# Performance work log

Hardware: AMD Instinct MI355X
Metric: run time of the kernel (lower is better)

Reference implementation:

```python
import jax, jax.numpy as jnp
import numpy as np
import math

EPS = 1e-12
SUPPORT = 1  # support_num
NEIGHBOR_NUM = 32

def _l2norm(x, axis):
    n = jnp.sqrt(jnp.sum(x * x, axis=axis, keepdims=True))
    return x / jnp.maximum(n, EPS)

def _sq_dist(a, b):
    # a: (bs, v1, 3), b: (bs, v2, 3) -> (bs, v1, v2)
    inner = jnp.einsum('bic,bjc->bij', a, b)
    a2 = jnp.sum(a * a, axis=-1)
    b2 = jnp.sum(b * b, axis=-1)
    return a2[:, :, None] + b2[:, None, :] - 2.0 * inner

def _knn(verts, k):
    d = _sq_dist(verts, verts)
    _, idx = jax.lax.top_k(-d, k + 1)
    return idx[:, :, 1:]  # drop self

def _gather(t, idx):
    # t: (bs, v, d), idx: (bs, ...) -> (bs, ..., d)
    return jax.vmap(lambda ti, ii: ti[ii])(t, idx)

def _dir_theta(nb_idx, verts, directions):
    nbr = _gather(verts, nb_idx) - verts[:, :, None, :]  # (bs, v, n, 3)
    nbr = _l2norm(nbr, -1)
    sup = _l2norm(directions, 0)  # (3, s*out)
    return jax.nn.relu(jnp.einsum('bvnc,ck->bvnk', nbr, sup))

def _conv_surface(nb_idx, verts, directions, kernel_num):
    theta = _dir_theta(nb_idx, verts, directions)
    bs, v, n, _ = theta.shape
    theta = theta.reshape(bs, v, n, SUPPORT, kernel_num)
    return jnp.sum(jnp.max(theta, axis=2), axis=2)  # (bs, v, kernel)

def _conv_layer(nb_idx, verts, fm, w, b, directions, out_ch):
    theta = _dir_theta(nb_idx, verts, directions)  # (bs, v, n, s*out)
    f = fm @ w + b  # (bs, v, (s+1)*out)
    center = f[..., :out_ch]
    supp_nb = _gather(f[..., out_ch:], nb_idx)  # (bs, v, n, s*out)
    bs, v, n, _ = theta.shape
    act = (theta * supp_nb).reshape(bs, v, n, SUPPORT, out_ch)
    return center + jnp.sum(jnp.max(act, axis=2), axis=2)

def _pool(verts, fm, sample_idx, nbk=4):
    nb = _knn(verts, nbk)
    pooled = jnp.max(_gather(fm, nb), axis=2)
    return verts[:, sample_idx, :], pooled[:, sample_idx, :]

def _nearest(target, source):
    return jnp.argmin(_sq_dist(target, source), axis=-1)  # (bs, v1)

def _forward(vertices, sample_idx1, sample_idx2, dir0, w1, b1, d1, w2, b2, d2,
             w3, b3, d3, w4, b4, d4, cw1, cb1, cw2, cb2, cw3, cb3):
    nb = _knn(vertices, NEIGHBOR_NUM)
    fm_0 = jax.nn.relu(_conv_surface(nb, vertices, dir0, 128))
    fm_1 = jax.nn.relu(_conv_layer(nb, vertices, fm_0, w1, b1, d1, 128))
    v_p1, fm_p1 = _pool(vertices, fm_1, sample_idx1)
    nb = _knn(v_p1, NEIGHBOR_NUM)
    fm_2 = jax.nn.relu(_conv_layer(nb, v_p1, fm_p1, w2, b2, d2, 256))
    fm_3 = jax.nn.relu(_conv_layer(nb, v_p1, fm_2, w3, b3, d3, 256))
    v_p2, fm_p2 = _pool(v_p1, fm_3, sample_idx2)
    nb = _knn(v_p2, NEIGHBOR_NUM)
    fm_4 = _conv_layer(nb, v_p2, fm_p2, w4, b4, d4, 512)  # no relu
    f_global = jnp.max(fm_4, axis=1)  # (bs, 512)
    near1 = _nearest(vertices, v_p1)
    near2 = _nearest(vertices, v_p2)
    fm_2u = _gather(fm_2, near1)
    fm_3u = _gather(fm_3, near1)
    fm_4u = _gather(fm_4, near2)
    bs, v = vertices.shape[0], vertices.shape[1]
    fg = jnp.broadcast_to(f_global[:, None, :], (bs, v, f_global.shape[-1]))
    fuse = jnp.concatenate([fm_0, fm_1, fm_2u, fm_3u, fm_4u, fg], axis=2)  # (bs, v, 1792)
    h = jax.nn.relu(jnp.einsum('bvc,oc->bvo', fuse, cw1) + cb1)
    h = jax.nn.relu(jnp.einsum('bvc,oc->bvo', h, cw2) + cb2)
    return jnp.einsum('bvc,oc->bvo', h, cw3) + cb3  # (bs, v, class_num)


def setup_inputs() -> dict:
    key = jax.random.key(0)
    ks = jax.random.split(key, 24)
    BS, N, CLS = 4, 4096, 13
    def u(k, shape, s):
        return jax.random.uniform(k, shape, jnp.float32, -s, s)
    inp = {}
    inp['vertices'] = jax.random.normal(ks[0], (BS, N, 3), jnp.float32)
    inp['sample_idx1'] = jax.random.permutation(ks[1], N)[:N // 4]
    inp['sample_idx2'] = jax.random.permutation(ks[2], N // 4)[:N // 16]
    inp['dir0'] = u(ks[3], (3, SUPPORT * 128), 1.0 / math.sqrt(SUPPORT * 128))
    def conv_params(k1, k2, k3, cin, cout):
        s = 1.0 / math.sqrt(cout * (SUPPORT + 1))
        return (u(k1, (cin, (SUPPORT + 1) * cout), s),
                u(k2, ((SUPPORT + 1) * cout,), s),
                u(k3, (3, SUPPORT * cout), s))
    inp['w1'], inp['b1'], inp['d1'] = conv_params(ks[4], ks[5], ks[6], 128, 128)
    inp['w2'], inp['b2'], inp['d2'] = conv_params(ks[7], ks[8], ks[9], 128, 256)
    inp['w3'], inp['b3'], inp['d3'] = conv_params(ks[10], ks[11], ks[12], 256, 256)
    inp['w4'], inp['b4'], inp['d4'] = conv_params(ks[13], ks[14], ks[15], 256, 512)
    DF = 1792
    inp['cw1'] = u(ks[16], (512, DF), 1.0 / math.sqrt(DF))
    inp['cb1'] = u(ks[17], (512,), 1.0 / math.sqrt(DF))
    inp['cw2'] = u(ks[18], (512, 512), 1.0 / math.sqrt(512))
    inp['cb2'] = u(ks[19], (512,), 1.0 / math.sqrt(512))
    inp['cw3'] = u(ks[20], (CLS, 512), 1.0 / math.sqrt(512))
    inp['cb3'] = u(ks[21], (CLS,), 1.0 / math.sqrt(512))
    return inp


def reference(vertices, sample_idx1, sample_idx2, dir0, w1, b1, d1, w2, b2, d2,
              w3, b3, d3, w4, b4, d4, cw1, cb1, cw2, cb2, cw3, cb3):
    return _forward(vertices, sample_idx1, sample_idx2, dir0, w1, b1, d1, w2, b2, d2,
                    w3, b3, d3, w4, b4, d4, cw1, cb1, cw2, cb2, cw3, cb3)
```

## Files before the change

kernel.cpp:

```cpp
#include <hip/hip_runtime.h>
#include <cstdint>
#include <cstddef>

namespace {

typedef unsigned short ushort_t;
typedef __bf16 bf16x8 __attribute__((ext_vector_type(8)));
typedef float  f32x4  __attribute__((ext_vector_type(4)));

constexpr int B_ = 4;
constexpr int N0 = 4096;
constexpr int N1 = 1024;
constexpr int N2 = 256;

__device__ __forceinline__ ushort_t f2bf_rne(float x) {
  uint32_t b = __float_as_uint(x);
  b += 0x7FFFu + ((b >> 16) & 1u);
  return (ushort_t)(b >> 16);
}
__device__ __forceinline__ float bf2f(ushort_t h) {
  return __uint_as_float(((uint32_t)h) << 16);
}
__device__ __forceinline__ void split_store(float x, ushort_t* hi, ushort_t* lo,
                                            size_t i) {
  const ushort_t h = f2bf_rne(x);
  hi[i] = h;
  lo[i] = f2bf_rne(x - bf2f(h));
}

__global__ void weight_prep_kernel(
    const float* __restrict__ w1, const float* __restrict__ w2,
    const float* __restrict__ w3, const float* __restrict__ w4,
    const float* __restrict__ cw1, const float* __restrict__ cw2,
    ushort_t* __restrict__ w1th, ushort_t* __restrict__ w1tl,
    ushort_t* __restrict__ w2th, ushort_t* __restrict__ w2tl,
    ushort_t* __restrict__ w3th, ushort_t* __restrict__ w3tl,
    ushort_t* __restrict__ w4th, ushort_t* __restrict__ w4tl,
    ushort_t* __restrict__ w1h, ushort_t* __restrict__ w1l,
    ushort_t* __restrict__ w2h, ushort_t* __restrict__ w2l)
{
  const int i = blockIdx.x * blockDim.x + threadIdx.x;
  if (i < 32768) {
    const int j = i, k = j % 128, n = j / 128;
    split_store(w1[(size_t)k * 256 + n], w1th, w1tl, (size_t)n * 128 + k);
  } else if (i < 98304) {
    const int j = i - 32768, k = j % 128, n = j / 128;
    split_store(w2[(size_t)k * 512 + n], w2th, w2tl, (size_t)n * 128 + k);
  } else if (i < 229376) {
    const int j = i - 98304, k = j % 256, n = j / 256;
    split_store(w3[(size_t)k * 512 + n], w3th, w3tl, (size_t)n * 256 + k);
  } else if (i < 491520) {
    const int j = i - 229376, k = j % 256, n = j / 256;
    split_store(w4[(size_t)k * 1024 + n], w4th, w4tl, (size_t)n * 256 + k);
  } else if (i < 1409024) {
    const int j = i - 491520;
    split_store(cw1[j], w1h, w1l, j);
  } else if (i < 1671168) {
    const int j = i - 1409024;
    split_store(cw2[j], w2h, w2l, j);
  }
}

__device__ __forceinline__ void bitonic_sort64(float& sd, int& si, int lane) {
#pragma unroll
  for (int kk = 2; kk <= 64; kk <<= 1) {
#pragma unroll
    for (int j = kk >> 1; j > 0; j >>= 1) {
      const float od = __shfl_xor(sd, j);
      const int   oi = __shfl_xor(si, j);
      const bool less    = (sd < od) || (sd == od && si < oi);
      const bool wantMin = ((lane & j) == 0) == ((lane & kk) == 0);
      if (wantMin != less) { sd = od; si = oi; }
    }
  }
}

__device__ __forceinline__ void knn_flush(float& ld, int& li, float& tau,
                                          int cnt, const float* bufd,
                                          const int* bufi, int lane, int Km1) {
  float sd = (lane < cnt) ? bufd[lane] : INFINITY;
  int   si = (lane < cnt) ? bufi[lane] : 0x7fffffff;
  bitonic_sort64(sd, si, lane);
  const float rd = __shfl(sd, 63 - lane);
  const int   ri = __shfl(si, 63 - lane);
  const bool keep = (ld < rd) || (ld == rd && li < ri);
  float md = keep ? ld : rd;
  int   mi = keep ? li : ri;
#pragma unroll
  for (int j = 32; j > 0; j >>= 1) {
    const float od = __shfl_xor(md, j);
    const int   oi = __shfl_xor(mi, j);
    const bool less    = (md < od) || (md == od && mi < oi);
    const bool wantMin = ((lane & j) == 0);
    if (wantMin != less) { md = od; mi = oi; }
  }
  ld = md; li = mi;
  tau = __shfl(ld, Km1);
}

template<int K, int TILE>
__launch_bounds__(512)
__global__ void knn_wave_kernel(const float* __restrict__ pts,
                                int Q, int C,
                                int* __restrict__ out)
{
  __shared__ float4 sp[TILE];
  __shared__ float sbd[8][64];
  __shared__ int   sbi[8][64];
  const int b    = blockIdx.y;
  const int lane = threadIdx.x & 63;
  const int wid  = threadIdx.x >> 6;
  const int q    = blockIdx.x * 8 + wid;
  const int self = q;
  const float* pb = pts + (size_t)b * C * 3;
  const float qx = pb[self * 3 + 0];
  const float qy = pb[self * 3 + 1];
  const float qz = pb[self * 3 + 2];
  const float q2   = qx * qx + qy * qy + qz * qz;
  const float m2qx = -2.0f * qx, m2qy = -2.0f * qy, m2qz = -2.0f * qz;

  float ld = INFINITY; int li = 0x7fffffff;
  float tau = INFINITY;
  int cnt = 0;
  float* bufd = sbd[wid];
  int*   bufi = sbi[wid];

  auto append = [&](unsigned long long m, bool cand, float d, int ci) {
    const int c = __popcll(m);
    if (cnt + c > 64) {
      knn_flush(ld, li, tau, cnt, bufd, bufi, lane, K - 1);
      cnt = 0;
    }
    const int prefix = __popcll(m & ((1ull << lane) - 1ull));
    if (cand) { bufd[cnt + prefix] = d; bufi[cnt + prefix] = ci; }
    cnt += c;
  };

  for (int t0 = 0; t0 < C; t0 += TILE) {
    __syncthreads();
    for (int i = threadIdx.x; i < TILE; i += 512) {
      const float x = pb[(t0 + i) * 3 + 0];
      const float y = pb[(t0 + i) * 3 + 1];
      const float z = pb[(t0 + i) * 3 + 2];
      sp[i] = make_float4(x, y, z, x * x + y * y + z * z);
    }
    __syncthreads();
    int base = 0;
    if (t0 == 0) {
      const float4 p = sp[lane];
      const float d = fmaf(m2qx, p.x, fmaf(m2qy, p.y, fmaf(m2qz, p.z, p.w + q2)));
      const bool valid = (lane != self);
      float sd = valid ? d : INFINITY;
      int   si = valid ? lane : 0x7fffffff;
      bitonic_sort64(sd, si, lane);
      ld = sd; li = si;
      tau = __shfl(ld, K - 1);
      base = 64;
    }
    for (; base + 128 <= TILE; base += 128) {
      const int ci0 = t0 + base + lane;
      const int ci1 = ci0 + 64;
      const float4 p0 = sp[base + lane];
      const float4 p1 = sp[base + 64 + lane];
      const float d0 = fmaf(m2qx, p0.x, fmaf(m2qy, p0.y, fmaf(m2qz, p0.z, p0.w + q2)));
      const float d1 = fmaf(m2qx, p1.x, fmaf(m2qy, p1.y, fmaf(m2qz, p1.z, p1.w + q2)));
      const bool c0 = (ci0 != self) && (d0 < tau);
      const bool c1 = (ci1 != self) && (d1 < tau);
      const unsigned long long m0 = __ballot(c0);
      const unsigned long long m1 = __ballot(c1);
      if (m0) append(m0, c0, d0, ci0);
      if (m1) append(m1, c1, d1, ci1);
    }
    if (base < TILE) {
      const int ci = t0 + base + lane;
      const float4 p = sp[base + lane];
      const float d = fmaf(m2qx, p.x, fmaf(m2qy, p.y, fmaf(m2qz, p.z, p.w + q2)));
      const bool c = (ci != self) && (d < tau);
      const unsigned long long m = __ballot(c);
      if (m) append(m, c, d, ci);
    }
  }
  if (cnt > 0) knn_flush(ld, li, tau, cnt, bufd, bufi, lane, K - 1);
  if (lane < K) out[((size_t)b * Q + q) * K + lane] = li;
}

__launch_bounds__(256)
__global__ void nearest_dual_kernel(const float* __restrict__ qpts,
                                    const float* __restrict__ cpts1,
                                    const float* __restrict__ cpts2,
                                    int* __restrict__ out1,
                                    int* __restrict__ out2)
{
  __shared__ float4 sp[1024];
  const int lvl = blockIdx.y;
  const int C = lvl ? N2 : N1;
  const float* cpts = lvl ? cpts2 : cpts1;
  int* out = lvl ? out2 : out1;
  const int lane = threadIdx.x & 63;
  const int wid  = threadIdx.x >> 6;
  const int q    = blockIdx.x * 4 + wid;
  const int b    = q >> 12;
  const float qx = qpts[(size_t)q * 3 + 0];
  const float qy = qpts[(size_t)q * 3 + 1];
  const float qz = qpts[(size_t)q * 3 + 2];
  const float q2   = qx * qx + qy * qy + qz * qz;
  const float m2qx = -2.0f * qx, m2qy = -2.0f * qy, m2qz = -2.0f * qz;
  const float* pb = cpts + (size_t)b * C * 3;

  for (int i = threadIdx.x; i < C; i += 256) {
    const float x = pb[i * 3 + 0];
    const float y = pb[i * 3 + 1];
    const float z = pb[i * 3 + 2];
    sp[i] = make_float4(x, y, z, x * x + y * y + z * z);
  }
  __syncthreads();
  float best = INFINITY; int bi = 0x7fffffff;
  for (int base = 0; base < C; base += 64) {
    const float4 p = sp[base + lane];
    const float d = fmaf(m2qx, p.x, fmaf(m2qy, p.y, fmaf(m2qz, p.z, p.w + q2)));
    if (d < best) { best = d; bi = base + lane; }
  }
#pragma unroll
  for (int j = 1; j < 64; j <<= 1) {
    const float od = __shfl_xor(best, j);
    const int   oi = __shfl_xor(bi, j);
    if (od < best || (od == best && oi < bi)) { best = od; bi = oi; }
  }
  if (lane == 0) out[q] = bi;
}

__global__ void conv_surface_kernel(const float* __restrict__ verts,
                                    const int*   __restrict__ nb,
                                    const float* __restrict__ dir,
                                    int V, int C,
                                    ushort_t* __restrict__ outH,
                                    ushort_t* __restrict__ outL) {
  __shared__ float ux[32], uy[32], uz[32];
  const int bv = blockIdx.x;
  const int b = bv / V;
  const int v = bv - b * V;
  const float* vb = verts + (size_t)b * V * 3;
  if (threadIdx.x < 32) {
    const float cx = vb[v * 3 + 0], cy = vb[v * 3 + 1], cz = vb[v * 3 + 2];
    const int nidx = nb[(size_t)bv * 32 + threadIdx.x];
    const float dx = vb[nidx * 3 + 0] - cx;
    const float dy = vb[nidx * 3 + 1] - cy;
    const float dz = vb[nidx * 3 + 2] - cz;
    const float rn = 1.0f / fmaxf(sqrtf(dx * dx + dy * dy + dz * dz), 1e-12f);
    ux[threadIdx.x] = dx * rn; uy[threadIdx.x] = dy * rn; uz[threadIdx.x] = dz * rn;
  }
  __syncthreads();
  const int o = threadIdx.x;
  float d0 = dir[o], d1 = dir[C + o], d2 = dir[2 * C + o];
  const float rn = 1.0f / fmaxf(sqrtf(d0 * d0 + d1 * d1 + d2 * d2), 1e-12f);
  d0 *= rn; d1 *= rn; d2 *= rn;
  float m = -INFINITY;
#pragma unroll
  for (int n = 0; n < 32; ++n) {
    const float t = fmaxf(0.0f, fmaf(d2, uz[n], fmaf(d1, uy[n], d0 * ux[n])));
    m = fmaxf(m, t);
  }
  split_store(fmaxf(0.0f, m), outH, outL, (size_t)bv * C + o);
}

__global__ void conv_combine_kernel(const float* __restrict__ f,
                                    const int*   __restrict__ nb,
                                    const float* __restrict__ dir,
                                    const float* __restrict__ verts,
                                    int V, int C, int relu,
                                    ushort_t* __restrict__ outH,
                                    ushort_t* __restrict__ outL) {
  __shared__ float ux[32], uy[32], uz[32];
  __shared__ int snb[32];
  const int bv = blockIdx.x;
  const int b = bv / V;
  const int v = bv - b * V;
  const float* vb = verts + (size_t)b * V * 3;
  if (threadIdx.x < 32) {
    const float cx = vb[v * 3 + 0], cy = vb[v * 3 + 1], cz = vb[v * 3 + 2];
    const int nidx = nb[(size_t)bv * 32 + threadIdx.x];
    snb[threadIdx.x] = nidx;
    const float dx = vb[nidx * 3 + 0] - cx;
    const float dy = vb[nidx * 3 + 1] - cy;
    const float dz = vb[nidx * 3 + 2] - cz;
    const float rn = 1.0f / fmaxf(sqrtf(dx * dx + dy * dy + dz * dz), 1e-12f);
    ux[threadIdx.x] = dx * rn; uy[threadIdx.x] = dy * rn; uz[threadIdx.x] = dz * rn;
  }
  __syncthreads();
  const int o = threadIdx.x;
  float d0 = dir[o], d1 = dir[C + o], d2 = dir[2 * C + o];
  const float rn = 1.0f / fmaxf(sqrtf(d0 * d0 + d1 * d1 + d2 * d2), 1e-12f);
  d0 *= rn; d1 *= rn; d2 *= rn;
  const float* fb = f + (size_t)b * V * 2 * C;
  float m = -INFINITY;
#pragma unroll 8
  for (int n = 0; n < 32; ++n) {
    const float t = fmaxf(0.0f, fmaf(d2, uz[n], fmaf(d1, uy[n], d0 * ux[n])));
    const float s = fb[(size_t)snb[n] * 2 * C + C + o];
    m = fmaxf(m, t * s);
  }
  float r = fb[(size_t)v * 2 * C + o] + m;
  if (relu) r = fmaxf(r, 0.0f);
  split_store(r, outH, outL, (size_t)bv * C + o);
}

__global__ void pool_kernel(const ushort_t* __restrict__ fmH,
                            const ushort_t* __restrict__ fmL,
                            const int*   __restrict__ nb,
                            const int*   __restrict__ sidx,
                            int Q, int Vsrc, int C,
                            ushort_t* __restrict__ outH,
                            ushort_t* __restrict__ outL) {
  const int i = blockIdx.x * blockDim.x + threadIdx.x;
  if (i >= B_ * Q * C) return;
  const int c = i % C;
  const int q = (i / C) % Q;
  const int b = i / (C * Q);
  const int* nn = nb + ((size_t)b * Vsrc + sidx[q]) * 32;
  const size_t fb = (size_t)b * Vsrc * C;
  float m = -INFINITY;
#pragma unroll
  for (int t = 0; t < 4; ++t) {
    const size_t idx = fb + (size_t)nn[t] * C + c;
    m = fmaxf(m, bf2f(fmH[idx]) + bf2f(fmL[idx]));
  }
  split_store(m, outH, outL, (size_t)i);
}

__global__ void gather_verts_kernel(const float* __restrict__ src,
                                    const int* __restrict__ idx,
                                    int Vsrc, int Q, float* __restrict__ dst) {
  const int i = blockIdx.x * blockDim.x + threadIdx.x;
  if (i >= B_ * Q * 3) return;
  const int c = i % 3;
  const int q = (i / 3) % Q;
  const int b = i / (3 * Q);
  dst[i] = src[((size_t)b * Vsrc + idx[q]) * 3 + c];
}

__global__ void global_max_kernel(const ushort_t* __restrict__ fmH,
                                  const ushort_t* __restrict__ fmL,
                                  ushort_t* __restrict__ outH,
                                  ushort_t* __restrict__ outL) {
  const int i = blockIdx.x * blockDim.x + threadIdx.x;
  if (i >= B_ * 512) return;
  const int c = i % 512;
  const int b = i / 512;
  const size_t base = (size_t)b * 256 * 512 + c;
  float m = -INFINITY;
  for (int v = 0; v < 256; ++v) {
    const size_t idx = base + (size_t)v * 512;
    m = fmaxf(m, bf2f(fmH[idx]) + bf2f(fmL[idx]));
  }
  split_store(m, outH, outL, (size_t)i);
}

constexpr int LDT = 40;

template<bool FUSE, bool SPLITOUT, bool RELU>
__launch_bounds__(256)
__global__ void mfma_gemm_kernel(
    const ushort_t* __restrict__ Ahi, const ushort_t* __restrict__ Alo,
    const ushort_t* __restrict__ f0h, const ushort_t* __restrict__ f0l,
    const ushort_t* __restrict__ f1h, const ushort_t* __restrict__ f1l,
    const ushort_t* __restrict__ f2h, const ushort_t* __restrict__ f2l,
    const ushort_t* __restrict__ f3h, const ushort_t* __restrict__ f3l,
    const ushort_t* __restrict__ f4h, const ushort_t* __restrict__ f4l,
    const ushort_t* __restrict__ fgh, const ushort_t* __restrict__ fgl,
    const int* __restrict__ near1, const int* __restrict__ near2,
    const ushort_t* __restrict__ Bhi, const ushort_t* __restrict__ Blo,
    const float* __restrict__ bias, int K,
    float* __restrict__ outF, ushort_t* __restrict__ outHi,
    ushort_t* __restrict__ outLo, int Nn)
{
  __shared__ ushort_t As_h[128 * LDT];
  __shared__ ushort_t As_l[128 * LDT];
  __shared__ ushort_t Bs_h[128 * LDT];
  __shared__ ushort_t Bs_l[128 * LDT];

  const int tid  = threadIdx.x;
  const int lane = tid & 63;
  const int wv   = tid >> 6;
  const int wr   = wv >> 1, wc = wv & 1;
  const int quad = lane >> 4, ml = lane & 15;
  const int m0 = blockIdx.y * 128, n0 = blockIdx.x * 128;

  const int r  = tid >> 1;
  const int hh = (tid & 1) * 16;

  int fb = 0, r1 = 0, r2 = 0;
  if (FUSE) {
    const int m = m0 + r;
    fb = m >> 12;
    r1 = near1[m];
    r2 = near2[m];
  }

  f32x4 acc[4][4];
#pragma unroll
  for (int i = 0; i < 4; ++i)
#pragma unroll
    for (int j = 0; j < 4; ++j) acc[i][j] = f32x4{0.f, 0.f, 0.f, 0.f};

  for (int k0 = 0; k0 < K; k0 += 32) {
    const int k = k0 + hh;
    uint4 a0h, a1h, a0l, a1l;
    {
      const ushort_t *sh, *sl; size_t off;
      if (FUSE) {
        const int m = m0 + r;
        if (k < 128)       { sh = f0h; sl = f0l; off = (size_t)m * 128 + k; }
        else if (k < 256)  { sh = f1h; sl = f1l; off = (size_t)m * 128 + (k - 128); }
        else if (k < 512)  { sh = f2h; sl = f2l; off = ((size_t)fb * 1024 + r1) * 256 + (k - 256); }
        else if (k < 768)  { sh = f3h; sl = f3l; off = ((size_t)fb * 1024 + r1) * 256 + (k - 512); }
        else if (k < 1280) { sh = f4h; sl = f4l; off = ((size_t)fb * 256 + r2) * 512 + (k - 768); }
        else               { sh = fgh; sl = fgl; off = (size_t)fb * 512 + (k - 1280); }
      } else {
        sh = Ahi; sl = Alo; off = (size_t)(m0 + r) * K + k;
      }
      a0h = *(const uint4*)(sh + off); a1h = *(const uint4*)(sh + off + 8);
      a0l = *(const uint4*)(sl + off); a1l = *(const uint4*)(sl + off + 8);
    }
    uint4 b0h, b1h, b0l, b1l;
    {
      const size_t off = (size_t)(n0 + r) * K + k;
      b0h = *(const uint4*)(Bhi + off); b1h = *(const uint4*)(Bhi + off + 8);
      b0l = *(const uint4*)(Blo + off); b1l = *(const uint4*)(Blo + off + 8);
    }
    __syncthreads();
    *(uint4*)&As_h[r * LDT + hh]     = a0h;
    *(uint4*)&As_h[r * LDT + hh + 8] = a1h;
    *(uint4*)&As_l[r * LDT + hh]     = a0l;
    *(uint4*)&As_l[r * LDT + hh + 8] = a1l;
    *(uint4*)&Bs_h[r * LDT + hh]     = b0h;
    *(uint4*)&Bs_h[r * LDT + hh + 8] = b1h;
    *(uint4*)&Bs_l[r * LDT + hh]     = b0l;
    *(uint4*)&Bs_l[r * LDT + hh + 8] = b1l;
    __syncthreads();

    bf16x8 ah[4], al[4], bh[4], bl[4];
#pragma unroll
    for (int i = 0; i < 4; ++i) {
      const int row = wr * 64 + i * 16 + ml;
      ah[i] = *(const bf16x8*)&As_h[row * LDT + quad * 8];
      al[i] = *(const bf16x8*)&As_l[row * LDT + quad * 8];
    }
#pragma unroll
    for (int j = 0; j < 4; ++j) {
      const int row = wc * 64 + j * 16 + ml;
      bh[j] = *(const bf16x8*)&Bs_h[row * LDT + quad * 8];
      bl[j] = *(const bf16x8*)&Bs_l[row * LDT + quad * 8];
    }
#pragma unroll
    for (int i = 0; i < 4; ++i)
#pragma unroll
      for (int j = 0; j < 4; ++j) {
        acc[i][j] = __builtin_amdgcn_mfma_f32_16x16x32_bf16(al[i], bh[j], acc[i][j], 0, 0, 0);
        acc[i][j] = __builtin_amdgcn_mfma_f32_16x16x32_bf16(ah[i], bl[j], acc[i][j], 0, 0, 0);
        acc[i][j] = __builtin_amdgcn_mfma_f32_16x16x32_bf16(ah[i], bh[j], acc[i][j], 0, 0, 0);
      }
  }

#pragma unroll
  for (int i = 0; i < 4; ++i)
#pragma unroll
    for (int j = 0; j < 4; ++j) {
      const int n = n0 + wc * 64 + j * 16 + ml;
      const float bv = bias[n];
#pragma unroll
      for (int reg = 0; reg < 4; ++reg) {
        const int m = m0 + wr * 64 + i * 16 + quad * 4 + reg;
        float r = acc[i][j][reg] + bv;
        if (RELU) r = fmaxf(r, 0.0f);
        if (SPLITOUT) {
          const ushort_t h = f2bf_rne(r);
          outHi[(size_t)m * Nn + n] = h;
          outLo[(size_t)m * Nn + n] = f2bf_rne(r - bf2f(h));
        } else {
          outF[(size_t)m * Nn + n] = r;
        }
      }
    }
}

__global__ void head_kernel(const float* __restrict__ h,
                            const float* __restrict__ cw,
                            const float* __restrict__ cb,
                            float* __restrict__ out) {
  const int i = blockIdx.x * blockDim.x + threadIdx.x;
  if (i >= B_ * N0 * 13) return;
  const int o = i % 13;
  const int row = i / 13;
  const float* hr = h + (size_t)row * 512;
  const float* wr = cw + (size_t)o * 512;
  float acc = cb[o];
  for (int k = 0; k < 512; ++k) acc = fmaf(hr[k], wr[k], acc);
  out[i] = acc;
}

}

extern "C" void kernel_launch(void* const* d_in, const int* in_sizes, int n_in,
                              void* d_out, int out_size, void* d_ws, size_t ws_size,
                              hipStream_t stream)
{
  const float* vertices = (const float*)d_in[0];
  const int*   sidx1    = (const int*)  d_in[1];
  const int*   sidx2    = (const int*)  d_in[2];
  const float* dir0     = (const float*)d_in[3];
  const float* w1 = (const float*)d_in[4];
  const float* b1 = (const float*)d_in[5];
  const float* d1 = (const float*)d_in[6];
  const float* w2 = (const float*)d_in[7];
  const float* b2 = (const float*)d_in[8];
  const float* d2 = (const float*)d_in[9];
  const float* w3 = (const float*)d_in[10];
  const float* b3 = (const float*)d_in[11];
  const float* d3 = (const float*)d_in[12];
  const float* w4 = (const float*)d_in[13];
  const float* b4 = (const float*)d_in[14];
  const float* d4 = (const float*)d_in[15];
  const float* cw1 = (const float*)d_in[16];
  const float* cb1 = (const float*)d_in[17];
  const float* cw2 = (const float*)d_in[18];
  const float* cb2 = (const float*)d_in[19];
  const float* cw3 = (const float*)d_in[20];
  const float* cb3 = (const float*)d_in[21];
  (void)in_sizes; (void)n_in; (void)out_size; (void)ws_size;

  char* ws = (char*)d_ws;
  size_t off = 0;
  auto alloc = [&](size_t bytes) -> void* {
    void* p = ws + off;
    off += (bytes + 255) & ~(size_t)255;
    return p;
  };

  int*   nb1   = (int*)  alloc((size_t)B_ * N0 * 32 * 4);
  int*   nb2   = (int*)  alloc((size_t)B_ * N1 * 32 * 4);
  int*   nb3   = (int*)  alloc((size_t)B_ * N2 * 32 * 4);
  float* vp1   = (float*)alloc((size_t)B_ * N1 * 3 * 4);
  float* vp2   = (float*)alloc((size_t)B_ * N2 * 3 * 4);
  int*   near1 = (int*)  alloc((size_t)B_ * N0 * 4);
  int*   near2 = (int*)  alloc((size_t)B_ * N0 * 4);
  float* h2    = (float*)alloc((size_t)B_ * N0 * 512 * 4);
  float* fbuf  = (float*)alloc((size_t)B_ * N0 * 256 * 4);

  const size_t nF0 = (size_t)B_ * N0 * 128;
  const size_t nP1 = (size_t)B_ * N1 * 128;
  const size_t nF2 = (size_t)B_ * N1 * 256;
  const size_t nP2 = (size_t)B_ * N2 * 256;
  const size_t nF4 = (size_t)B_ * N2 * 512;
  const size_t nFg = (size_t)B_ * 512;
  const size_t nW1 = (size_t)512 * 1792;
  const size_t nW2 = (size_t)512 * 512;
  const size_t nH1 = (size_t)B_ * N0 * 512;
  ushort_t* f0h = (ushort_t*)alloc(nF0 * 2); ushort_t* f0l = (ushort_t*)alloc(nF0 * 2);
  ushort_t* f1h = (ushort_t*)alloc(nF0 * 2); ushort_t* f1l = (ushort_t*)alloc(nF0 * 2);
  ushort_t* p1h = (ushort_t*)alloc(nP1 * 2); ushort_t* p1l = (ushort_t*)alloc(nP1 * 2);
  ushort_t* f2h = (ushort_t*)alloc(nF2 * 2); ushort_t* f2l = (ushort_t*)alloc(nF2 * 2);
  ushort_t* f3h = (ushort_t*)alloc(nF2 * 2); ushort_t* f3l = (ushort_t*)alloc(nF2 * 2);
  ushort_t* p2h = (ushort_t*)alloc(nP2 * 2); ushort_t* p2l = (ushort_t*)alloc(nP2 * 2);
  ushort_t* f4h = (ushort_t*)alloc(nF4 * 2); ushort_t* f4l = (ushort_t*)alloc(nF4 * 2);
  ushort_t* fgh = (ushort_t*)alloc(nFg * 2); ushort_t* fgl = (ushort_t*)alloc(nFg * 2);
  ushort_t* w1h = (ushort_t*)alloc(nW1 * 2); ushort_t* w1l = (ushort_t*)alloc(nW1 * 2);
  ushort_t* w2h = (ushort_t*)alloc(nW2 * 2); ushort_t* w2l = (ushort_t*)alloc(nW2 * 2);
  ushort_t* h1h = (ushort_t*)alloc(nH1 * 2); ushort_t* h1l = (ushort_t*)alloc(nH1 * 2);
  ushort_t* w1th = (ushort_t*)alloc((size_t)256 * 128 * 2);
  ushort_t* w1tl = (ushort_t*)alloc((size_t)256 * 128 * 2);
  ushort_t* w2th = (ushort_t*)alloc((size_t)512 * 128 * 2);
  ushort_t* w2tl = (ushort_t*)alloc((size_t)512 * 128 * 2);
  ushort_t* w3th = (ushort_t*)alloc((size_t)512 * 256 * 2);
  ushort_t* w3tl = (ushort_t*)alloc((size_t)512 * 256 * 2);
  ushort_t* w4th = (ushort_t*)alloc((size_t)1024 * 256 * 2);
  ushort_t* w4tl = (ushort_t*)alloc((size_t)1024 * 256 * 2);

  const dim3 blk256(256), blk512(512);
  auto mgemm = [&](const ushort_t* Ah, const ushort_t* Al,
                   const ushort_t* Bh, const ushort_t* Bl, const float* bias,
                   int M, int Nn, int K, float* outF) {
    const dim3 grid(Nn / 128, M / 128);
    mfma_gemm_kernel<false, false, false><<<grid, blk256, 0, stream>>>(
        Ah, Al, nullptr, nullptr, nullptr, nullptr, nullptr, nullptr, nullptr,
        nullptr, nullptr, nullptr, nullptr, nullptr, nullptr, nullptr,
        Bh, Bl, bias, K, outF, nullptr, nullptr, Nn);
  };

  weight_prep_kernel<<<dim3(6528), blk256, 0, stream>>>(
      w1, w2, w3, w4, cw1, cw2,
      w1th, w1tl, w2th, w2tl, w3th, w3tl, w4th, w4tl,
      w1h, w1l, w2h, w2l);

  knn_wave_kernel<32, 2048><<<dim3(N0 / 8, B_), blk512, 0, stream>>>(vertices, N0, N0, nb1);
  conv_surface_kernel<<<dim3(B_ * N0), dim3(128), 0, stream>>>(
      vertices, nb1, dir0, N0, 128, f0h, f0l);
  mgemm(f0h, f0l, w1th, w1tl, b1, B_ * N0, 256, 128, fbuf);
  conv_combine_kernel<<<dim3(B_ * N0), dim3(128), 0, stream>>>(
      fbuf, nb1, d1, vertices, N0, 128, 1, f1h, f1l);

  gather_verts_kernel<<<dim3((B_ * N1 * 3 + 255) / 256), blk256, 0, stream>>>(vertices, sidx1, N0, N1, vp1);
  pool_kernel<<<dim3((B_ * N1 * 128 + 255) / 256), blk256, 0, stream>>>(
      f1h, f1l, nb1, sidx1, N1, N0, 128, p1h, p1l);

  knn_wave_kernel<32, 1024><<<dim3(N1 / 8, B_), blk512, 0, stream>>>(vp1, N1, N1, nb2);
  mgemm(p1h, p1l, w2th, w2tl, b2, B_ * N1, 512, 128, fbuf);
  conv_combine_kernel<<<dim3(B_ * N1), dim3(256), 0, stream>>>(
      fbuf, nb2, d2, vp1, N1, 256, 1, f2h, f2l);
  mgemm(f2h, f2l, w3th, w3tl, b3, B_ * N1, 512, 256, fbuf);
  conv_combine_kernel<<<dim3(B_ * N1), dim3(256), 0, stream>>>(
      fbuf, nb2, d3, vp1, N1, 256, 1, f3h, f3l);

  gather_verts_kernel<<<dim3((B_ * N2 * 3 + 255) / 256), blk256, 0, stream>>>(vp1, sidx2, N1, N2, vp2);
  pool_kernel<<<dim3((B_ * N2 * 256 + 255) / 256), blk256, 0, stream>>>(
      f3h, f3l, nb2, sidx2, N2, N1, 256, p2h, p2l);

  knn_wave_kernel<32, 256><<<dim3(N2 / 8, B_), blk512, 0, stream>>>(vp2, N2, N2, nb3);
  mgemm(p2h, p2l, w4th, w4tl, b4, B_ * N2, 1024, 256, fbuf);
  conv_combine_kernel<<<dim3(B_ * N2), dim3(512), 0, stream>>>(
      fbuf, nb3, d4, vp2, N2, 512, 0, f4h, f4l);
  global_max_kernel<<<dim3((B_ * 512 + 255) / 256), blk256, 0, stream>>>(
      f4h, f4l, fgh, fgl);

  nearest_dual_kernel<<<dim3((B_ * N0) / 4, 2), blk256, 0, stream>>>(
      vertices, vp1, vp2, near1, near2);

  mfma_gemm_kernel<true, true, true><<<dim3(512 / 128, (B_ * N0) / 128), blk256, 0, stream>>>(
      nullptr, nullptr,
      f0h, f0l, f1h, f1l, f2h, f2l, f3h, f3l, f4h, f4l, fgh, fgl,
      near1, near2, w1h, w1l, cb1, 1792, nullptr, h1h, h1l, 512);
  mfma_gemm_kernel<false, false, true><<<dim3(512 / 128, (B_ * N0) / 128), blk256, 0, stream>>>(
      h1h, h1l,
      nullptr, nullptr, nullptr, nullptr, nullptr, nullptr, nullptr, nullptr,
      nullptr, nullptr, nullptr, nullptr,
      nullptr, nullptr, w2h, w2l, cb2, 512, h2, nullptr, nullptr, 512);
  head_kernel<<<dim3((B_ * N0 * 13 + 255) / 256), blk256, 0, stream>>>(h2, cw3, cb3, (float*)d_out);
}
```

Before: 690.2 us.

## Use async global-to-LDS loads in GEMM, widen kNN blocks, parallelize reductions

The MFMA GEMM now loads tiles straight into LDS with global_load_lds, one wave per operand (A hi/lo, B hi/lo), in a k-chunked layout that replaces the padded register-staged copy. The kNN kernel moves from 512 to 1024 threads per block so each block handles 16 queries and shares each candidate tile across more waves. The global max reduction splits its vertex loop over four slices per channel and combines them in shared memory, and the head kernel reads float4. Together these aim to cut load latency and under-parallelized reductions, at the cost of no padding against LDS bank conflicts and higher register pressure in kNN at 1024 threads.

Result: slower. 756.0 us (+9.5%).

```diff
diff --git a/kernel.cpp b/kernel.cpp
--- a/kernel.cpp
+++ b/kernel.cpp
@@ -26,6 +26,12 @@
   const ushort_t h = f2bf_rne(x);
   hi[i] = h;
   lo[i] = f2bf_rne(x - bf2f(h));
+}
+
+__device__ __forceinline__ void async_copy16(const ushort_t* g, ushort_t* l) {
+  __builtin_amdgcn_global_load_lds(
+      (const __attribute__((address_space(1))) void*)g,
+      (__attribute__((address_space(3))) void*)l, 16, 0, 0);
 }
 
 __global__ void weight_prep_kernel(
@@ -99,18 +105,18 @@
 }
 
 template<int K, int TILE>
-__launch_bounds__(512)
+__launch_bounds__(1024)
 __global__ void knn_wave_kernel(const float* __restrict__ pts,
                                 int Q, int C,
                                 int* __restrict__ out)
 {
   __shared__ float4 sp[TILE];
-  __shared__ float sbd[8][64];
-  __shared__ int   sbi[8][64];
+  __shared__ float sbd[16][64];
+  __shared__ int   sbi[16][64];
   const int b    = blockIdx.y;
   const int lane = threadIdx.x & 63;
   const int wid  = threadIdx.x >> 6;
-  const int q    = blockIdx.x * 8 + wid;
+  const int q    = blockIdx.x * 16 + wid;
   const int self = q;
   const float* pb = pts + (size_t)b * C * 3;
   const float qx = pb[self * 3 + 0];
@@ -138,7 +144,7 @@
 
   for (int t0 = 0; t0 < C; t0 += TILE) {
     __syncthreads();
-    for (int i = threadIdx.x; i < TILE; i += 512) {
+    for (int i = threadIdx.x; i < TILE; i += 1024) {
       const float x = pb[(t0 + i) * 3 + 0];
       const float y = pb[(t0 + i) * 3 + 1];
       const float z = pb[(t0 + i) * 3 + 2];
@@ -342,20 +348,24 @@
                                   const ushort_t* __restrict__ fmL,
                                   ushort_t* __restrict__ outH,
                                   ushort_t* __restrict__ outL) {
-  const int i = blockIdx.x * blockDim.x + threadIdx.x;
-  if (i >= B_ * 512) return;
-  const int c = i % 512;
-  const int b = i / 512;
+  __shared__ float red[4][64];
+  const int t = threadIdx.x;
+  const int cl = t & 63, slice = t >> 6;
+  const int c = (blockIdx.x & 7) * 64 + cl;
+  const int b = blockIdx.x >> 3;
   const size_t base = (size_t)b * 256 * 512 + c;
   float m = -INFINITY;
-  for (int v = 0; v < 256; ++v) {
+  for (int v = slice; v < 256; v += 4) {
     const size_t idx = base + (size_t)v * 512;
     m = fmaxf(m, bf2f(fmH[idx]) + bf2f(fmL[idx]));
   }
-  split_store(m, outH, outL, (size_t)i);
-}
-
-constexpr int LDT = 40;
+  red[slice][cl] = m;
+  __syncthreads();
+  if (slice == 0) {
+    m = fmaxf(fmaxf(red[0][cl], red[1][cl]), fmaxf(red[2][cl], red[3][cl]));
+    split_store(m, outH, outL, (size_t)b * 512 + c);
+  }
+}
 
 template<bool FUSE, bool SPLITOUT, bool RELU>
 __launch_bounds__(256)
@@ -373,10 +383,10 @@
     float* __restrict__ outF, ushort_t* __restrict__ outHi,
     ushort_t* __restrict__ outLo, int Nn)
 {
-  __shared__ ushort_t As_h[128 * LDT];
-  __shared__ ushort_t As_l[128 * LDT];
-  __shared__ ushort_t Bs_h[128 * LDT];
-  __shared__ ushort_t Bs_l[128 * LDT];
+  __shared__ ushort_t As_h[4 * 128 * 8];
+  __shared__ ushort_t As_l[4 * 128 * 8];
+  __shared__ ushort_t Bs_h[4 * 128 * 8];
+  __shared__ ushort_t Bs_l[4 * 128 * 8];
 
   const int tid  = threadIdx.x;
   const int lane = tid & 63;
@@ -385,16 +395,16 @@
   const int quad = lane >> 4, ml = lane & 15;
   const int m0 = blockIdx.y * 128, n0 = blockIdx.x * 128;
 
-  const int r  = tid >> 1;
-  const int hh = (tid & 1) * 16;
-
-  int fb = 0, r1 = 0, r2 = 0;
+  int fb = 0, r1a = 0, r1b = 0, r2a = 0, r2b = 0;
   if (FUSE) {
-    const int m = m0 + r;
-    fb = m >> 12;
-    r1 = near1[m];
-    r2 = near2[m];
-  }
+    fb = m0 >> 12;
+    r1a = near1[m0 + lane];      r1b = near1[m0 + 64 + lane];
+    r2a = near2[m0 + lane];      r2b = near2[m0 + 64 + lane];
+  }
+  ushort_t* const tgt = (wv == 0) ? As_h : (wv == 1) ? As_l
+                       : (wv == 2) ? Bs_h : Bs_l;
+  const bool isA = (wv < 2);
+  const bool isHi = ((wv & 1) == 0);
 
   f32x4 acc[4][4];
 #pragma unroll
@@ -403,53 +413,47 @@
     for (int j = 0; j < 4; ++j) acc[i][j] = f32x4{0.f, 0.f, 0.f, 0.f};
 
   for (int k0 = 0; k0 < K; k0 += 32) {
-    const int k = k0 + hh;
-    uint4 a0h, a1h, a0l, a1l;
-    {
-      const ushort_t *sh, *sl; size_t off;
-      if (FUSE) {
-        const int m = m0 + r;
-        if (k < 128)       { sh = f0h; sl = f0l; off = (size_t)m * 128 + k; }
-        else if (k < 256)  { sh = f1h; sl = f1l; off = (size_t)m * 128 + (k - 128); }
-        else if (k < 512)  { sh = f2h; sl = f2l; off = ((size_t)fb * 1024 + r1) * 256 + (k - 256); }
-        else if (k < 768)  { sh = f3h; sl = f3l; off = ((size_t)fb * 1024 + r1) * 256 + (k - 512); }
-        else if (k < 1280) { sh = f4h; sl = f4l; off = ((size_t)fb * 256 + r2) * 512 + (k - 768); }
-        else               { sh = fgh; sl = fgl; off = (size_t)fb * 512 + (k - 1280); }
-      } else {
-        sh = Ahi; sl = Alo; off = (size_t)(m0 + r) * K + k;
+    __syncthreads();
+#pragma unroll
+    for (int h = 0; h < 2; ++h) {
+#pragma unroll
+      for (int c = 0; c < 4; ++c) {
+        const int k = k0 + c * 8;
+        const ushort_t* src;
+        if (!isA) {
+          src = (isHi ? Bhi : Blo) + (size_t)(n0 + h * 64 + lane) * K + k;
+        } else if (!FUSE) {
+          src = (isHi ? Ahi : Alo) + (size_t)(m0 + h * 64 + lane) * K + k;
+        } else {
+          const int m = m0 + h * 64 + lane;
+          const int rr1 = h ? r1b : r1a;
+          const int rr2 = h ? r2b : r2a;
+          const ushort_t* bp; size_t off;
+          if (k < 128)       { bp = isHi ? f0h : f0l; off = (size_t)m * 128 + k; }
+          else if (k < 256)  { bp = isHi ? f1h : f1l; off = (size_t)m * 128 + (k - 128); }
+          else if (k < 512)  { bp = isHi ? f2h : f2l; off = ((size_t)fb * 1024 + rr1) * 256 + (k - 256); }
+          else if (k < 768)  { bp = isHi ? f3h : f3l; off = ((size_t)fb * 1024 + rr1) * 256 + (k - 512); }
+          else if (k < 1280) { bp = isHi ? f4h : f4l; off = ((size_t)fb * 256 + rr2) * 512 + (k - 768); }
+          else               { bp = isHi ? fgh : fgl; off = (size_t)fb * 512 + (k - 1280); }
+          src = bp + off;
+        }
+        async_copy16(src, &tgt[c * 1024 + h * 512]);
       }
-      a0h = *(const uint4*)(sh + off); a1h = *(const uint4*)(sh + off + 8);
-      a0l = *(const uint4*)(sl + off); a1l = *(const uint4*)(sl + off + 8);
-    }
-    uint4 b0h, b1h, b0l, b1l;
-    {
-      const size_t off = (size_t)(n0 + r) * K + k;
-      b0h = *(const uint4*)(Bhi + off); b1h = *(const uint4*)(Bhi + off + 8);
-      b0l = *(const uint4*)(Blo + off); b1l = *(const uint4*)(Blo + off + 8);
-    }
-    __syncthreads();
-    *(uint4*)&As_h[r * LDT + hh]     = a0h;
-    *(uint4*)&As_h[r * LDT + hh + 8] = a1h;
-    *(uint4*)&As_l[r * LDT + hh]     = a0l;
-    *(uint4*)&As_l[r * LDT + hh + 8] = a1l;
-    *(uint4*)&Bs_h[r * LDT + hh]     = b0h;
-    *(uint4*)&Bs_h[r * LDT + hh + 8] = b1h;
-    *(uint4*)&Bs_l[r * LDT + hh]     = b0l;
-    *(uint4*)&Bs_l[r * LDT + hh + 8] = b1l;
+    }
     __syncthreads();
 
     bf16x8 ah[4], al[4], bh[4], bl[4];
 #pragma unroll
     for (int i = 0; i < 4; ++i) {
       const int row = wr * 64 + i * 16 + ml;
-      ah[i] = *(const bf16x8*)&As_h[row * LDT + quad * 8];
-      al[i] = *(const bf16x8*)&As_l[row * LDT + quad * 8];
+      ah[i] = *(const bf16x8*)&As_h[quad * 1024 + row * 8];
+      al[i] = *(const bf16x8*)&As_l[quad * 1024 + row * 8];
     }
 #pragma unroll
     for (int j = 0; j < 4; ++j) {
       const int row = wc * 64 + j * 16 + ml;
-      bh[j] = *(const bf16x8*)&Bs_h[row * LDT + quad * 8];
-      bl[j] = *(const bf16x8*)&Bs_l[row * LDT + quad * 8];
+      bh[j] = *(const bf16x8*)&Bs_h[quad * 1024 + row * 8];
+      bl[j] = *(const bf16x8*)&Bs_l[quad * 1024 + row * 8];
     }
 #pragma unroll
     for (int i = 0; i < 4; ++i)
@@ -491,10 +495,13 @@
   if (i >= B_ * N0 * 13) return;
   const int o = i % 13;
   const int row = i / 13;
-  const float* hr = h + (size_t)row * 512;
-  const float* wr = cw + (size_t)o * 512;
+  const float4* hr = (const float4*)(h + (size_t)row * 512);
+  const float4* wr = (const float4*)(cw + (size_t)o * 512);
   float acc = cb[o];
-  for (int k = 0; k < 512; ++k) acc = fmaf(hr[k], wr[k], acc);
+  for (int k = 0; k < 128; ++k) {
+    const float4 a = hr[k], w = wr[k];
+    acc = fmaf(a.x, w.x, fmaf(a.y, w.y, fmaf(a.z, w.z, fmaf(a.w, w.w, acc))));
+  }
   out[i] = acc;
 }
 
@@ -575,7 +582,7 @@
   ushort_t* w4th = (ushort_t*)alloc((size_t)1024 * 256 * 2);
   ushort_t* w4tl = (ushort_t*)alloc((size_t)1024 * 256 * 2);
 
-  const dim3 blk256(256), blk512(512);
+  const dim3 blk256(256), blk1024(1024);
   auto mgemm = [&](const ushort_t* Ah, const ushort_t* Al,
                    const ushort_t* Bh, const ushort_t* Bl, const float* bias,
                    int M, int Nn, int K, float* outF) {
@@ -591,7 +598,7 @@
       w1th, w1tl, w2th, w2tl, w3th, w3tl, w4th, w4tl,
       w1h, w1l, w2h, w2l);
 
-  knn_wave_kernel<32, 2048><<<dim3(N0 / 8, B_), blk512, 0, stream>>>(vertices, N0, N0, nb1);
+  knn_wave_kernel<32, 2048><<<dim3(N0 / 16, B_), blk1024, 0, stream>>>(vertices, N0, N0, nb1);
   conv_surface_kernel<<<dim3(B_ * N0), dim3(128), 0, stream>>>(
       vertices, nb1, dir0, N0, 128, f0h, f0l);
   mgemm(f0h, f0l, w1th, w1tl, b1, B_ * N0, 256, 128, fbuf);
@@ -602,7 +609,7 @@
   pool_kernel<<<dim3((B_ * N1 * 128 + 255) / 256), blk256, 0, stream>>>(
       f1h, f1l, nb1, sidx1, N1, N0, 128, p1h, p1l);
 
-  knn_wave_kernel<32, 1024><<<dim3(N1 / 8, B_), blk512, 0, stream>>>(vp1, N1, N1, nb2);
+  knn_wave_kernel<32, 1024><<<dim3(N1 / 16, B_), blk1024, 0, stream>>>(vp1, N1, N1, nb2);
   mgemm(p1h, p1l, w2th, w2tl, b2, B_ * N1, 512, 128, fbuf);
   conv_combine_kernel<<<dim3(B_ * N1), dim3(256), 0, stream>>>(
       fbuf, nb2, d2, vp1, N1, 256, 1, f2h, f2l);
@@ -614,12 +621,11 @@
   pool_kernel<<<dim3((B_ * N2 * 256 + 255) / 256), blk256, 0, stream>>>(
       f3h, f3l, nb2, sidx2, N2, N1, 256, p2h, p2l);
 
-  knn_wave_kernel<32, 256><<<dim3(N2 / 8, B_), blk512, 0, stream>>>(vp2, N2, N2, nb3);
+  knn_wave_kernel<32, 256><<<dim3(N2 / 16, B_), blk1024, 0, stream>>>(vp2, N2, N2, nb3);
   mgemm(p2h, p2l, w4th, w4tl, b4, B_ * N2, 1024, 256, fbuf);
   conv_combine_kernel<<<dim3(B_ * N2), dim3(512), 0, stream>>>(
       fbuf, nb3, d4, vp2, N2, 512, 0, f4h, f4l);
-  global_max_kernel<<<dim3((B_ * 512 + 255) / 256), blk256, 0, stream>>>(
-      f4h, f4l, fgh, fgl);
+  global_max_kernel<<<dim3(B_ * 8), blk256, 0, stream>>>(f4h, f4l, fgh, fgl);
 
   nearest_dual_kernel<<<dim3((B_ * N0) / 4, 2), blk256, 0, stream>>>(
       vertices, vp1, vp2, near1, near2);
```

## Widen KNN blocks, split global max reduction, vectorize head loads

Applied to the files above, without the earlier changes.

The KNN kernel now runs 16 query waves per 1024-thread block instead of 8, so each loaded candidate tile is shared by more queries and fewer tiles are staged in total. The global max kernel splits each channel's 256-row reduction across four thread slices and combines them in shared memory, which raises parallelism for a small reduction. The head kernel reads activations and weights as float4, so it issues fewer load instructions. Larger KNN blocks use more registers and LDS per block and may lower occupancy, and the float4 reorder changes the order of floating-point accumulation.

Result: faster. 666.5 us (-3.4%).

```diff
diff --git a/kernel.cpp b/kernel.cpp
--- a/kernel.cpp
+++ b/kernel.cpp
@@ -99,18 +99,18 @@
 }
 
 template<int K, int TILE>
-__launch_bounds__(512)
+__launch_bounds__(1024)
 __global__ void knn_wave_kernel(const float* __restrict__ pts,
                                 int Q, int C,
                                 int* __restrict__ out)
 {
   __shared__ float4 sp[TILE];
-  __shared__ float sbd[8][64];
-  __shared__ int   sbi[8][64];
+  __shared__ float sbd[16][64];
+  __shared__ int   sbi[16][64];
   const int b    = blockIdx.y;
   const int lane = threadIdx.x & 63;
   const int wid  = threadIdx.x >> 6;
-  const int q    = blockIdx.x * 8 + wid;
+  const int q    = blockIdx.x * 16 + wid;
   const int self = q;
   const float* pb = pts + (size_t)b * C * 3;
   const float qx = pb[self * 3 + 0];
@@ -138,7 +138,7 @@
 
   for (int t0 = 0; t0 < C; t0 += TILE) {
     __syncthreads();
-    for (int i = threadIdx.x; i < TILE; i += 512) {
+    for (int i = threadIdx.x; i < TILE; i += 1024) {
       const float x = pb[(t0 + i) * 3 + 0];
       const float y = pb[(t0 + i) * 3 + 1];
       const float z = pb[(t0 + i) * 3 + 2];
@@ -342,17 +342,23 @@
                                   const ushort_t* __restrict__ fmL,
                                   ushort_t* __restrict__ outH,
                                   ushort_t* __restrict__ outL) {
-  const int i = blockIdx.x * blockDim.x + threadIdx.x;
-  if (i >= B_ * 512) return;
-  const int c = i % 512;
-  const int b = i / 512;
+  __shared__ float red[4][64];
+  const int t = threadIdx.x;
+  const int cl = t & 63, slice = t >> 6;
+  const int c = (blockIdx.x & 7) * 64 + cl;
+  const int b = blockIdx.x >> 3;
   const size_t base = (size_t)b * 256 * 512 + c;
   float m = -INFINITY;
-  for (int v = 0; v < 256; ++v) {
+  for (int v = slice; v < 256; v += 4) {
     const size_t idx = base + (size_t)v * 512;
     m = fmaxf(m, bf2f(fmH[idx]) + bf2f(fmL[idx]));
   }
-  split_store(m, outH, outL, (size_t)i);
+  red[slice][cl] = m;
+  __syncthreads();
+  if (slice == 0) {
+    m = fmaxf(fmaxf(red[0][cl], red[1][cl]), fmaxf(red[2][cl], red[3][cl]));
+    split_store(m, outH, outL, (size_t)b * 512 + c);
+  }
 }
 
 constexpr int LDT = 40;
@@ -491,10 +497,13 @@
   if (i >= B_ * N0 * 13) return;
   const int o = i % 13;
   const int row = i / 13;
-  const float* hr = h + (size_t)row * 512;
-  const float* wr = cw + (size_t)o * 512;
+  const float4* hr = (const float4*)(h + (size_t)row * 512);
+  const float4* wr = (const float4*)(cw + (size_t)o * 512);
   float acc = cb[o];
-  for (int k = 0; k < 512; ++k) acc = fmaf(hr[k], wr[k], acc);
+  for (int k = 0; k < 128; ++k) {
+    const float4 a = hr[k], w = wr[k];
+    acc = fmaf(a.x, w.x, fmaf(a.y, w.y, fmaf(a.z, w.z, fmaf(a.w, w.w, acc))));
+  }
   out[i] = acc;
 }
 
@@ -575,7 +584,7 @@
   ushort_t* w4th = (ushort_t*)alloc((size_t)1024 * 256 * 2);
   ushort_t* w4tl = (ushort_t*)alloc((size_t)1024 * 256 * 2);
 
-  const dim3 blk256(256), blk512(512);
+  const dim3 blk256(256), blk1024(1024);
   auto mgemm = [&](const ushort_t* Ah, const ushort_t* Al,
                    const ushort_t* Bh, const ushort_t* Bl, const float* bias,
                    int M, int Nn, int K, float* outF) {
@@ -591,7 +600,7 @@
       w1th, w1tl, w2th, w2tl, w3th, w3tl, w4th, w4tl,
       w1h, w1l, w2h, w2l);
 
-  knn_wave_kernel<32, 2048><<<dim3(N0 / 8, B_), blk512, 0, stream>>>(vertices, N0, N0, nb1);
+  knn_wave_kernel<32, 2048><<<dim3(N0 / 16, B_), blk1024, 0, stream>>>(vertices, N0, N0, nb1);
   conv_surface_kernel<<<dim3(B_ * N0), dim3(128), 0, stream>>>(
       vertices, nb1, dir0, N0, 128, f0h, f0l);
   mgemm(f0h, f0l, w1th, w1tl, b1, B_ * N0, 256, 128, fbuf);
@@ -602,7 +611,7 @@
   pool_kernel<<<dim3((B_ * N1 * 128 + 255) / 256), blk256, 0, stream>>>(
       f1h, f1l, nb1, sidx1, N1, N0, 128, p1h, p1l);
 
-  knn_wave_kernel<32, 1024><<<dim3(N1 / 8, B_), blk512, 0, stream>>>(vp1, N1, N1, nb2);
+  knn_wave_kernel<32, 1024><<<dim3(N1 / 16, B_), blk1024, 0, stream>>>(vp1, N1, N1, nb2);
   mgemm(p1h, p1l, w2th, w2tl, b2, B_ * N1, 512, 128, fbuf);
   conv_combine_kernel<<<dim3(B_ * N1), dim3(256), 0, stream>>>(
       fbuf, nb2, d2, vp1, N1, 256, 1, f2h, f2l);
@@ -614,12 +623,11 @@
   pool_kernel<<<dim3((B_ * N2 * 256 + 255) / 256), blk256, 0, stream>>>(
       f3h, f3l, nb2, sidx2, N2, N1, 256, p2h, p2l);
 
-  knn_wave_kernel<32, 256><<<dim3(N2 / 8, B_), blk512, 0, stream>>>(vp2, N2, N2, nb3);
+  knn_wave_kernel<32, 256><<<dim3(N2 / 16, B_), blk1024, 0, stream>>>(vp2, N2, N2, nb3);
   mgemm(p2h, p2l, w4th, w4tl, b4, B_ * N2, 1024, 256, fbuf);
   conv_combine_kernel<<<dim3(B_ * N2), dim3(512), 0, stream>>>(
       fbuf, nb3, d4, vp2, N2, 512, 0, f4h, f4l);
-  global_max_kernel<<<dim3((B_ * 512 + 255) / 256), blk256, 0, stream>>>(
-      f4h, f4l, fgh, fgl);
+  global_max_kernel<<<dim3(B_ * 8), blk256, 0, stream>>>(f4h, f4l, fgh, fgl);
 
   nearest_dual_kernel<<<dim3((B_ * N0) / 4, 2), blk256, 0, stream>>>(
       vertices, vp1, vp2, near1, near2);
```
